# Kernel optimization log

Measured on AMD Instinct MI355X. Metric: run time of the kernel, lower is better.

## Reference

```python
import jax, jax.numpy as jnp
import numpy as np

INPUT_DIM = 1024
LATENT_DIM = 1024


def setup_inputs() -> dict:
    key = jax.random.key(0)
    ks = jax.random.split(key, 8)
    B, T = 64, 512
    concat_dim = INPUT_DIM + LATENT_DIM
    s = lambda fan_in: 1.0 / np.sqrt(fan_in)
    return {
        "x": jax.random.normal(ks[0], (B, T, INPUT_DIM), dtype=jnp.float32),
        "h0": jax.random.normal(ks[1], (B, LATENT_DIM), dtype=jnp.float32),
        "w_W": jax.random.uniform(ks[2], (concat_dim, 2 * LATENT_DIM), jnp.float32, -s(concat_dim), s(concat_dim)),
        "w_b": jax.random.uniform(ks[3], (2 * LATENT_DIM,), jnp.float32, -s(concat_dim), s(concat_dim)),
        "wx_W": jax.random.uniform(ks[4], (INPUT_DIM, LATENT_DIM), jnp.float32, -s(INPUT_DIM), s(INPUT_DIM)),
        "wx_b": jax.random.uniform(ks[5], (LATENT_DIM,), jnp.float32, -s(INPUT_DIM), s(INPUT_DIM)),
        "wh_W": jax.random.uniform(ks[6], (LATENT_DIM, LATENT_DIM), jnp.float32, -s(LATENT_DIM), s(LATENT_DIM)),
        "wh_b": jax.random.uniform(ks[7], (LATENT_DIM,), jnp.float32, -s(LATENT_DIM), s(LATENT_DIM)),
    }


def reference(x, h0, w_W, w_b, wx_W, wx_b, wh_W, wh_b):
    # x: [B, T, D_in] (batch_first). Scan over time.
    xT = jnp.swapaxes(x, 0, 1)  # [T, B, D_in]

    def step(h, x_t):
        # fused gate: sigmoid(cat([x,h]) @ W + b) -> chunk into hidden/output gates
        fused = jax.nn.sigmoid(jnp.concatenate([x_t, h], axis=-1) @ w_W + w_b)
        hidden_state, output_state = jnp.split(fused, 2, axis=-1)
        memory_state = (x_t @ wx_W + wx_b) + hidden_state * (h @ wh_W + wh_b)
        h_new = output_state * h + (1.0 - output_state) * jnp.tanh(memory_state)
        return h_new, h_new

    _, hs = jax.lax.scan(step, h0, xT)  # hs: [T, B, L]
    return jnp.swapaxes(hs, 0, 1)  # [B, T, L]
```

## Files before the change

### kernel.cpp

```cpp
#include <hip/hip_runtime.h>
#include <hip/hip_bf16.h>


typedef __attribute__((ext_vector_type(4))) int   int4v;
typedef __attribute__((ext_vector_type(4))) short short4v;
typedef __attribute__((ext_vector_type(8))) short bf16x8;
typedef __attribute__((ext_vector_type(4))) float f32x4;

union Pack16 { int4v i; short4v s[2]; };
union FragU  { bf16x8 v; short4v s[2]; int4v i; };

__device__ __forceinline__ short f2bf(float f) {
  union { float f; unsigned u; } v; v.f = f;
  unsigned r = v.u + 0x7fffu + ((v.u >> 16) & 1u);
  return (short)(r >> 16);
}
__device__ __forceinline__ float bf2f(short s) {
  union { unsigned u; float f; } v; v.u = ((unsigned)(unsigned short)s) << 16;
  return v.f;
}

#define LDS_BARRIER()                                         \
  do {                                                        \
    asm volatile("s_waitcnt lgkmcnt(0)" ::: "memory");        \
    __builtin_amdgcn_s_barrier();                             \
    asm volatile("" ::: "memory");                            \
  } while (0)


__global__ __launch_bounds__(256) void cast_x_kernel(const float* __restrict__ xf,
                                                     short* __restrict__ xbf, int n4) {
  int i = blockIdx.x * 256 + threadIdx.x;
  if (i < n4) {
    float4 v = ((const float4*)xf)[i];
    short4v o;
    o.x = f2bf(v.x); o.y = f2bf(v.y); o.z = f2bf(v.z); o.w = f2bf(v.w);
    int r_in = i >> 8, c = i & 255;
    int b = r_in >> 9, t = r_in & 511;
    ((short4v*)xbf)[((t << 6) + b) * 256 + c] = o;
  }
}

__global__ __launch_bounds__(256) void transpose_cast(const float* __restrict__ src,
                                                      long ld, short* __restrict__ dst) {
  __shared__ float tile[64][65];
  const int n0 = blockIdx.x << 6, k0 = blockIdx.y << 6;
  const int c = threadIdx.x & 63, rr = threadIdx.x >> 6;
#pragma unroll 4
  for (int i = 0; i < 16; ++i)
    tile[i * 4 + rr][c] = src[(long)(k0 + i * 4 + rr) * ld + n0 + c];
  __syncthreads();
#pragma unroll 4
  for (int i = 0; i < 16; ++i)
    dst[(long)(n0 + i * 4 + rr) * 1024 + k0 + c] = f2bf(tile[c][i * 4 + rr]);
}

__global__ __launch_bounds__(256) void prep_misc(const float* __restrict__ wb,
                                                 const float* __restrict__ wxb,
                                                 const float* __restrict__ h0,
                                                 float* __restrict__ biasP,
                                                 short* __restrict__ hbf0) {
  int i = blockIdx.x * 256 + threadIdx.x;
  if (i < 65536) {
    hbf0[i] = f2bf(h0[i]);
  } else {
    int n = i - 65536;
    if (n < 3072) biasP[n] = (n < 2048) ? wb[n] : wxb[n - 2048];
  }
}

__global__ __launch_bounds__(256) void pgemm_kernel(const short* __restrict__ A,
                                                    const short* __restrict__ Bt,
                                                    const float* __restrict__ biasP,
                                                    short* __restrict__ P) {
  __shared__ short As[128][36];
  __shared__ short Bs[128][36];
  const int tid = threadIdx.x;
  const int m0 = blockIdx.y << 7;
  const int n0 = blockIdx.x << 7;
  const int w = tid >> 6, lane = tid & 63;
  const int wm = w >> 1, wn = w & 1;
  const int q = lane >> 4, r = lane & 15;
  const int srow = tid >> 1, shalf = tid & 1;

  const f32x4 zero = {0.f, 0.f, 0.f, 0.f};
  f32x4 acc[4][4];
#pragma unroll
  for (int a = 0; a < 4; ++a)
#pragma unroll
    for (int b = 0; b < 4; ++b) acc[a][b] = zero;

  const short* gA = A + (long)(m0 + srow) * 1024 + shalf * 16;
  const short* gB = Bt + (long)(n0 + srow) * 1024 + shalf * 16;

  for (int kk = 0; kk < 1024; kk += 32) {
    Pack16 a0, a1, b0, b1;
    a0.i = *(const int4v*)(gA + kk);
    a1.i = *(const int4v*)(gA + kk + 8);
    b0.i = *(const int4v*)(gB + kk);
    b1.i = *(const int4v*)(gB + kk + 8);
    short* wA = &As[srow][shalf * 16];
    *(short4v*)(wA)      = a0.s[0];
    *(short4v*)(wA + 4)  = a0.s[1];
    *(short4v*)(wA + 8)  = a1.s[0];
    *(short4v*)(wA + 12) = a1.s[1];
    short* wB = &Bs[srow][shalf * 16];
    *(short4v*)(wB)      = b0.s[0];
    *(short4v*)(wB + 4)  = b0.s[1];
    *(short4v*)(wB + 8)  = b1.s[0];
    *(short4v*)(wB + 12) = b1.s[1];
    __syncthreads();

    FragU af[4], bfv[4];
#pragma unroll
    for (int mi = 0; mi < 4; ++mi) {
      const short* pa = &As[wm * 64 + mi * 16 + r][q * 8];
      af[mi].s[0] = *(const short4v*)pa;
      af[mi].s[1] = *(const short4v*)(pa + 4);
    }
#pragma unroll
    for (int ni = 0; ni < 4; ++ni) {
      const short* pb = &Bs[wn * 64 + ni * 16 + r][q * 8];
      bfv[ni].s[0] = *(const short4v*)pb;
      bfv[ni].s[1] = *(const short4v*)(pb + 4);
    }
#pragma unroll
    for (int mi = 0; mi < 4; ++mi)
#pragma unroll
      for (int ni = 0; ni < 4; ++ni)
        acc[mi][ni] = __builtin_amdgcn_mfma_f32_16x16x32_bf16(af[mi].v, bfv[ni].v,
                                                              acc[mi][ni], 0, 0, 0);
    __syncthreads();
  }

#pragma unroll
  for (int ni = 0; ni < 4; ++ni) {
    int gn = n0 + wn * 64 + ni * 16 + r;
    float bias = biasP[gn];
#pragma unroll
    for (int mi = 0; mi < 4; ++mi) {
      int gm = m0 + wm * 64 + mi * 16 + q * 4;
#pragma unroll
      for (int i = 0; i < 4; ++i)
        P[(long)(gm + i) * 3072 + gn] = f2bf(acc[mi][ni][i] + bias);
    }
  }
}

__global__ __launch_bounds__(256, 1) void recur_kernel(const short* __restrict__ RT,
                                                       const short* __restrict__ P,
                                                       const float* __restrict__ whb,
                                                       const float* __restrict__ h0,
                                                       short* __restrict__ hbuf,
                                                       float* __restrict__ out,
                                                       unsigned* __restrict__ sync) {
  __shared__ float Lred[4][3][256];
  __shared__ unsigned long long hstage_u[32];
  short* hstage = (short*)hstage_u;

  const int tid = threadIdx.x;
  const int bid = blockIdx.x;
  const int cg = bid & 63, bg = bid >> 6;
  const int w = tid >> 6, lane = tid & 63;
  const int q = lane >> 4, r = lane & 15;
  const int ks = w << 8;
  const f32x4 zero = {0.f, 0.f, 0.f, 0.f};

  FragU Bf[3][8];
#pragma unroll
  for (int nt = 0; nt < 3; ++nt)
#pragma unroll
    for (int ki = 0; ki < 8; ++ki) {
      const short* p = RT + (long)(nt * 1024 + cg * 16 + r) * 1024 + ks + ki * 32 + q * 8;
      Pack16 t16; t16.i = *(const int4v*)p;
      Bf[nt][ki].s[0] = t16.s[0]; Bf[nt][ki].s[1] = t16.s[1];
    }

  const int bl = tid >> 4, jl = tid & 15;
  float hp = h0[(long)(bg * 16 + bl) * 1024 + cg * 16 + jl];
  const float whbr = whb[cg * 16 + jl];
  const short* Pbase = P + (long)(bg * 16 + bl) * 3072 + cg * 16 + jl;
  short p0n = Pbase[0], p1n = Pbase[1024], p2n = Pbase[2048];
  const long outbase = ((long)(bg * 16 + bl) * 512) * 1024 + cg * 16 + jl;

  unsigned* ctr = sync + bg * 32;
  unsigned* gf  = sync + 128 + bg * 32;

  for (int t = 0; t < 512; ++t) {
    const short* hcur = hbuf + (t & 1) * 65536;
    short* hnext = hbuf + ((t + 1) & 1) * 65536;

    const short* aptr = hcur + (bg * 16 + r) * 1024 + ks + q * 8;
    FragU Af[8];
    asm volatile(
        "global_load_dwordx4 %0, %8, off sc0 sc1\n\t"
        "global_load_dwordx4 %1, %8, off offset:64 sc0 sc1\n\t"
        "global_load_dwordx4 %2, %8, off offset:128 sc0 sc1\n\t"
        "global_load_dwordx4 %3, %8, off offset:192 sc0 sc1\n\t"
        "global_load_dwordx4 %4, %8, off offset:256 sc0 sc1\n\t"
        "global_load_dwordx4 %5, %8, off offset:320 sc0 sc1\n\t"
        "global_load_dwordx4 %6, %8, off offset:384 sc0 sc1\n\t"
        "global_load_dwordx4 %7, %8, off offset:448 sc0 sc1\n\t"
        "s_waitcnt vmcnt(0)"
        : "=&v"(Af[0].i), "=&v"(Af[1].i), "=&v"(Af[2].i), "=&v"(Af[3].i),
          "=&v"(Af[4].i), "=&v"(Af[5].i), "=&v"(Af[6].i), "=&v"(Af[7].i)
        : "v"(aptr)
        : "memory");

    short c0 = p0n, c1 = p1n, c2 = p2n;
    if (t < 511) {
      const short* Pn = Pbase + (long)(t + 1) * 196608;
      p0n = Pn[0]; p1n = Pn[1024]; p2n = Pn[2048];
    }

    f32x4 acc0 = zero, acc1 = zero, acc2 = zero;
#pragma unroll
    for (int ki = 0; ki < 8; ++ki) {
      acc0 = __builtin_amdgcn_mfma_f32_16x16x32_bf16(Af[ki].v, Bf[0][ki].v, acc0, 0, 0, 0);
      acc1 = __builtin_amdgcn_mfma_f32_16x16x32_bf16(Af[ki].v, Bf[1][ki].v, acc1, 0, 0, 0);
      acc2 = __builtin_amdgcn_mfma_f32_16x16x32_bf16(Af[ki].v, Bf[2][ki].v, acc2, 0, 0, 0);
    }

#pragma unroll
    for (int i = 0; i < 4; ++i) {
      Lred[w][0][(q * 4 + i) * 16 + r] = acc0[i];
      Lred[w][1][(q * 4 + i) * 16 + r] = acc1[i];
      Lred[w][2][(q * 4 + i) * 16 + r] = acc2[i];
    }
    LDS_BARRIER();

    float g0 = Lred[0][0][tid] + Lred[1][0][tid] + Lred[2][0][tid] + Lred[3][0][tid];
    float g1 = Lred[0][1][tid] + Lred[1][1][tid] + Lred[2][1][tid] + Lred[3][1][tid];
    float g2 = Lred[0][2][tid] + Lred[1][2][tid] + Lred[2][2][tid] + Lred[3][2][tid];

    float gh = 1.f / (1.f + __expf(-(bf2f(c0) + g0)));
    float go = 1.f / (1.f + __expf(-(bf2f(c1) + g1)));
    float mem = bf2f(c2) + gh * (g2 + whbr);
    float e = __expf(2.f * mem);
    float th = 1.f - 2.f / (e + 1.f);
    float hn = go * hp + (1.f - go) * th;
    hp = hn;
    out[outbase + (long)t * 1024] = hn;
    hstage[tid] = f2bf(hn);
    LDS_BARRIER();

    if (tid < 64) {
      int row = bg * 16 + (tid >> 2);
      unsigned long long* hp64 = (unsigned long long*)(hnext + row * 1024 + cg * 16 + (tid & 3) * 4);
      __hip_atomic_store(hp64, hstage_u[tid], __ATOMIC_RELAXED, __HIP_MEMORY_SCOPE_AGENT);
      asm volatile("s_waitcnt vmcnt(0)" ::: "memory");
      if (tid == 0) {
        unsigned old = __hip_atomic_fetch_add(ctr, 1u, __ATOMIC_RELAXED,
                                              __HIP_MEMORY_SCOPE_AGENT);
        if (old == 64u * (unsigned)(t + 1) - 1u)
          __hip_atomic_store(gf, (unsigned)(t + 1), __ATOMIC_RELAXED,
                             __HIP_MEMORY_SCOPE_AGENT);
      }
    }
    while (__hip_atomic_load(gf, __ATOMIC_RELAXED, __HIP_MEMORY_SCOPE_AGENT) <
           (unsigned)(t + 1))
      __builtin_amdgcn_s_sleep(1);
  }
}


extern "C" void kernel_launch(void* const* d_in, const int* in_sizes, int n_in,
                              void* d_out, int out_size, void* d_ws, size_t ws_size,
                              hipStream_t stream) {
  const float* x   = (const float*)d_in[0];
  const float* h0  = (const float*)d_in[1];
  const float* wW  = (const float*)d_in[2];
  const float* wb  = (const float*)d_in[3];
  const float* wxW = (const float*)d_in[4];
  const float* wxb = (const float*)d_in[5];
  const float* whW = (const float*)d_in[6];
  const float* whb = (const float*)d_in[7];
  float* out = (float*)d_out;

  char* ws = (char*)d_ws;
  short*    P     = (short*)(ws);
  short*    xbf   = (short*)(ws + 201326592);
  short*    XwT   = (short*)(ws + 268435456);
  short*    RT    = (short*)(ws + 274726912);
  float*    biasP = (float*)(ws + 281018368);
  short*    hbf   = (short*)(ws + 281030656);
  unsigned* sync  = (unsigned*)(ws + 281292800);

  hipMemsetAsync(sync, 0, 1024, stream);
  cast_x_kernel<<<dim3(32768), dim3(256), 0, stream>>>(x, xbf, 8388608);
  transpose_cast<<<dim3(32, 16), dim3(256), 0, stream>>>(wW, 2048, XwT);
  transpose_cast<<<dim3(16, 16), dim3(256), 0, stream>>>(wxW, 1024, XwT + 2048 * 1024);
  transpose_cast<<<dim3(32, 16), dim3(256), 0, stream>>>(wW + 1024 * 2048, 2048, RT);
  transpose_cast<<<dim3(16, 16), dim3(256), 0, stream>>>(whW, 1024, RT + 2048 * 1024);
  prep_misc<<<dim3(268), dim3(256), 0, stream>>>(wb, wxb, h0, biasP, hbf);
  pgemm_kernel<<<dim3(24, 256), dim3(256), 0, stream>>>(xbf, XwT, biasP, P);
  recur_kernel<<<dim3(256), dim3(256), 0, stream>>>(RT, P, whb, h0, hbf, out, sync);
}
```

Baseline: 2.588 ms.

## Use direct global-to-LDS loads in pgemm and single-wave grid barrier spin

New measurement: 2.490 ms. -3.8%, faster.

```diff
diff --git a/kernel.cpp b/kernel.cpp
--- a/kernel.cpp
+++ b/kernel.cpp
@@ -26,6 +26,12 @@
     __builtin_amdgcn_s_barrier();                             \
     asm volatile("" ::: "memory");                            \
   } while (0)
+
+__device__ __forceinline__ void gload_lds16(const short* g, short* l) {
+  __builtin_amdgcn_global_load_lds(
+      (const __attribute__((address_space(1))) void*)g,
+      (__attribute__((address_space(3))) void*)l, 16, 0, 0);
+}
 
 
 __global__ __launch_bounds__(256) void cast_x_kernel(const float* __restrict__ xf,
@@ -73,15 +79,25 @@
                                                     const short* __restrict__ Bt,
                                                     const float* __restrict__ biasP,
                                                     short* __restrict__ P) {
-  __shared__ short As[128][36];
-  __shared__ short Bs[128][36];
+  __shared__ short As[128][32];
+  __shared__ short Bs[128][32];
   const int tid = threadIdx.x;
   const int m0 = blockIdx.y << 7;
   const int n0 = blockIdx.x << 7;
   const int w = tid >> 6, lane = tid & 63;
   const int wm = w >> 1, wn = w & 1;
   const int q = lane >> 4, r = lane & 15;
-  const int srow = tid >> 1, shalf = tid & 1;
+
+  const int srow = (w << 5) + (lane >> 2);
+  const int scol = (lane & 3) * 8;
+  const short* gA0 = A  + (long)(m0 + srow) * 1024 + scol;
+  const short* gA1 = gA0 + 16 * 1024;
+  const short* gB0 = Bt + (long)(n0 + srow) * 1024 + scol;
+  const short* gB1 = gB0 + 16 * 1024;
+  short* lA0 = &As[(w << 5)][0];
+  short* lA1 = &As[(w << 5) + 16][0];
+  short* lB0 = &Bs[(w << 5)][0];
+  short* lB1 = &Bs[(w << 5) + 16][0];
 
   const f32x4 zero = {0.f, 0.f, 0.f, 0.f};
   f32x4 acc[4][4];
@@ -90,40 +106,20 @@
 #pragma unroll
     for (int b = 0; b < 4; ++b) acc[a][b] = zero;
 
-  const short* gA = A + (long)(m0 + srow) * 1024 + shalf * 16;
-  const short* gB = Bt + (long)(n0 + srow) * 1024 + shalf * 16;
-
   for (int kk = 0; kk < 1024; kk += 32) {
-    Pack16 a0, a1, b0, b1;
-    a0.i = *(const int4v*)(gA + kk);
-    a1.i = *(const int4v*)(gA + kk + 8);
-    b0.i = *(const int4v*)(gB + kk);
-    b1.i = *(const int4v*)(gB + kk + 8);
-    short* wA = &As[srow][shalf * 16];
-    *(short4v*)(wA)      = a0.s[0];
-    *(short4v*)(wA + 4)  = a0.s[1];
-    *(short4v*)(wA + 8)  = a1.s[0];
-    *(short4v*)(wA + 12) = a1.s[1];
-    short* wB = &Bs[srow][shalf * 16];
-    *(short4v*)(wB)      = b0.s[0];
-    *(short4v*)(wB + 4)  = b0.s[1];
-    *(short4v*)(wB + 8)  = b1.s[0];
-    *(short4v*)(wB + 12) = b1.s[1];
+    gload_lds16(gA0 + kk, lA0);
+    gload_lds16(gA1 + kk, lA1);
+    gload_lds16(gB0 + kk, lB0);
+    gload_lds16(gB1 + kk, lB1);
     __syncthreads();
 
     FragU af[4], bfv[4];
 #pragma unroll
-    for (int mi = 0; mi < 4; ++mi) {
-      const short* pa = &As[wm * 64 + mi * 16 + r][q * 8];
-      af[mi].s[0] = *(const short4v*)pa;
-      af[mi].s[1] = *(const short4v*)(pa + 4);
-    }
-#pragma unroll
-    for (int ni = 0; ni < 4; ++ni) {
-      const short* pb = &Bs[wn * 64 + ni * 16 + r][q * 8];
-      bfv[ni].s[0] = *(const short4v*)pb;
-      bfv[ni].s[1] = *(const short4v*)(pb + 4);
-    }
+    for (int mi = 0; mi < 4; ++mi)
+      af[mi].i = *(const int4v*)&As[wm * 64 + mi * 16 + r][q * 8];
+#pragma unroll
+    for (int ni = 0; ni < 4; ++ni)
+      bfv[ni].i = *(const int4v*)&Bs[wn * 64 + ni * 16 + r][q * 8];
 #pragma unroll
     for (int mi = 0; mi < 4; ++mi)
 #pragma unroll
@@ -256,10 +252,11 @@
           __hip_atomic_store(gf, (unsigned)(t + 1), __ATOMIC_RELAXED,
                              __HIP_MEMORY_SCOPE_AGENT);
       }
-    }
-    while (__hip_atomic_load(gf, __ATOMIC_RELAXED, __HIP_MEMORY_SCOPE_AGENT) <
-           (unsigned)(t + 1))
-      __builtin_amdgcn_s_sleep(1);
+      while (__hip_atomic_load(gf, __ATOMIC_RELAXED, __HIP_MEMORY_SCOPE_AGENT) <
+             (unsigned)(t + 1))
+        __builtin_amdgcn_s_sleep(1);
+    }
+    LDS_BARRIER();
   }
 }
 
```
